# Optimization experiments

Measured on AMD Instinct MI355X. Metric: run time of the kernel, lower is better.

Reference implementation:

```python
import jax, jax.numpy as jnp
import numpy as np

NUM_HEADS = 4
LN_EPS = 1e-5


def setup_inputs() -> dict:
    key = jax.random.key(0)
    B, S, D = 4, 2048, 1024
    H = NUM_HEADS
    hd = D // H
    ks = jax.random.split(key, 8)
    s = 1.0 / np.sqrt(hd)
    inp = {
        "embeddings": jax.random.normal(ks[0], (B, S, D), dtype=jnp.float32),
        # per-head Q/K/V projection weights (torch Linear weight layout [out,in])
        "Wq": jax.random.normal(ks[1], (H, hd, hd), dtype=jnp.float32) * s,
        "Wk": jax.random.normal(ks[2], (H, hd, hd), dtype=jnp.float32) * s,
        "Wv": jax.random.normal(ks[3], (H, hd, hd), dtype=jnp.float32) * s,
        # lens bias scalars: causal, intent, temporal, normative (init values from module)
        "bias_scalars": jnp.array([0.1, 0.15, 0.05, 0.2], dtype=jnp.float32),
        "Wo_w": jax.random.normal(ks[4], (D, D), dtype=jnp.float32) / np.sqrt(D),
        "Wo_b": jnp.zeros((D,), dtype=jnp.float32),
        "ln_g": jnp.ones((D,), dtype=jnp.float32),
        "ln_b": jnp.zeros((D,), dtype=jnp.float32),
    }
    return inp


def _legal_biases(x, bias_scalars):
    """x: [B,H,S,hd] per-head embeddings. Returns stacked bias [B,H,S,S]."""
    B, H, S, hd = x.shape
    # head 0: CAUSAL -> strictly upper triangular mask * causal_bias
    causal = jnp.triu(jnp.ones((S, S), dtype=x.dtype), k=1)  # [S,S]
    b0 = causal[None] * bias_scalars[0]                      # [1,S,S] -> bcast B
    b0 = jnp.broadcast_to(b0, (B, S, S))
    # head 1: INTENTIONALITY -> outer product of embedding norms, global-mean threshold
    mag1 = jnp.linalg.norm(x[:, 1], axis=-1)                 # [B,S]
    intent = mag1[:, :, None] * mag1[:, None, :]             # [B,S,S]
    b1 = (intent > intent.mean()).astype(x.dtype) * bias_scalars[1]
    # head 2: TEMPORAL -> exp(-|i-j|/S)
    pos = jnp.arange(S, dtype=x.dtype)
    prox = jnp.exp(-jnp.abs(pos[:, None] - pos[None, :]) / S)  # [S,S]
    b2 = jnp.broadcast_to(prox[None] * bias_scalars[2], (B, S, S))
    # head 3: NORMATIVE -> outer product of last feature, > 0.5 threshold
    v3 = x[:, 3, :, -1]                                      # [B,S]
    viol = v3[:, :, None] * v3[:, None, :]                   # [B,S,S]
    b3 = (viol > 0.5).astype(x.dtype) * bias_scalars[3]
    return jnp.stack([b0, b1, b2, b3], axis=1)               # [B,H,S,S]


def _forward(embeddings, Wq, Wk, Wv, bias_scalars, Wo_w, Wo_b, ln_g, ln_b):
    B, S, D = embeddings.shape
    H = NUM_HEADS
    hd = D // H
    x = embeddings.reshape(B, S, H, hd).transpose(0, 2, 1, 3)     # [B,H,S,hd]
    # torch Linear: y = x @ W.T
    Q = jnp.einsum('bhsd,hed->bhse', x, Wq)
    K = jnp.einsum('bhsd,hed->bhse', x, Wk)
    V = jnp.einsum('bhsd,hed->bhse', x, Wv)
    scores = jnp.einsum('bhse,bhte->bhst', Q, K) / np.sqrt(hd)    # [B,H,S,S]
    scores = scores + _legal_biases(x, bias_scalars)
    weights = jax.nn.softmax(scores, axis=-1)                     # [B,H,S,S]
    attended = jnp.einsum('bhst,bhte->bhse', weights, V)          # [B,H,S,hd]
    concat = attended.transpose(0, 2, 1, 3).reshape(B, S, D)      # head order = concat order
    out = concat @ Wo_w.T + Wo_b
    # layer_norm(out + embeddings)
    y = out + embeddings
    mu = y.mean(axis=-1, keepdims=True)
    var = ((y - mu) ** 2).mean(axis=-1, keepdims=True)
    output = (y - mu) / jnp.sqrt(var + LN_EPS) * ln_g + ln_b      # [B,S,D]
    average_weights = weights.mean(axis=1)                        # [B,S,S]
    guilt = jax.nn.softmax(average_weights.sum(axis=-1), axis=-1) # [B,S]
    return output, average_weights, guilt


def reference(embeddings, Wq, Wk, Wv, bias_scalars, Wo_w, Wo_b, ln_g, ln_b):
    return _forward(embeddings, Wq, Wk, Wv, bias_scalars, Wo_w, Wo_b, ln_g, ln_b)
```

## Files before the change

kernel.cpp:

```cpp
#include <hip/hip_runtime.h>
#include <hip/hip_bf16.h>
#include <math.h>

#define S_ 2048
#define D_ 1024
#define H_ 4
#define HD_ 256
#define B_ 4

typedef __hip_bfloat16 bf16;
typedef short s16x8 __attribute__((ext_vector_type(8)));
typedef short s16x4 __attribute__((ext_vector_type(4)));
typedef float f32x4 __attribute__((ext_vector_type(4)));

#define GLOAD16(g, l)                                             \
    __builtin_amdgcn_global_load_lds(                             \
        (const __attribute__((address_space(1))) void*)(g),       \
        (__attribute__((address_space(3))) void*)(l), 16, 0, 0)

#define PLOAD(dst, p)                                             \
    asm volatile("global_load_dwordx4 %0, %1, off"                \
                 : "=&v"(dst) : "v"(p) : "memory")

static __device__ inline short bfb(float x) {
    bf16 t = __float2bfloat16(x);
    short s;
    __builtin_memcpy(&s, &t, 2);
    return s;
}

template <int MODE>
__global__ __launch_bounds__(256) void mfma_nt(
    int K,
    const bf16* __restrict__ A, int lda, long sA_b, long sA_h,
    const bf16* __restrict__ Bm, int ldb, long sB_b, long sB_h,
    void* __restrict__ Cp, int ldc, long sC_b, long sC_h,
    int zdiv, int bbase,
    const double* __restrict__ mag1d, const double* __restrict__ v3d,
    const double* __restrict__ meand, const float* __restrict__ bias_sc)
{
    __shared__ __align__(16) short As[128 * 32];
    __shared__ __align__(16) short Bs[128 * 32];

    const int tid = threadIdx.x;
    const int w = tid >> 6, lane = tid & 63;
    const int srow = lane >> 2;
    const int scol = (((lane & 3) ^ (srow & 3)) << 3);
    const int quad = lane >> 4, r = lane & 15;
    const int qx = quad ^ (r & 3);
    const int wr = (w >> 1) * 64, wc = (w & 1) * 64;
    const int zb = blockIdx.z / zdiv, zh = blockIdx.z % zdiv;

    const bf16* Ap = A + (size_t)zb * sA_b + (size_t)zh * sA_h +
                     (size_t)blockIdx.y * 128 * lda;
    const bf16* Bp = Bm + (size_t)zb * sB_b + (size_t)zh * sB_h +
                     (size_t)blockIdx.x * 128 * ldb;

    f32x4 acc[4][4] = {};

    for (int k0 = 0; k0 < K; k0 += 32) {
        if (k0) __syncthreads();
#pragma unroll
        for (int l = 0; l < 2; l++) {
            GLOAD16(Ap + (size_t)(w * 32 + l * 16 + srow) * lda + (k0 + scol),
                    &As[(w * 32 + l * 16) * 32]);
            GLOAD16(Bp + (size_t)(w * 32 + l * 16 + srow) * ldb + (k0 + scol),
                    &Bs[(w * 32 + l * 16) * 32]);
        }
        __syncthreads();

        s16x8 af[4], bfv[4];
        const s16x8* A8 = (const s16x8*)As;
        const s16x8* B8 = (const s16x8*)Bs;
#pragma unroll
        for (int i = 0; i < 4; i++) af[i] = A8[(wr + i * 16 + r) * 4 + qx];
#pragma unroll
        for (int j = 0; j < 4; j++) bfv[j] = B8[(wc + j * 16 + r) * 4 + qx];
#pragma unroll
        for (int i = 0; i < 4; i++)
#pragma unroll
            for (int j = 0; j < 4; j++)
                acc[i][j] = __builtin_amdgcn_mfma_f32_16x16x32_bf16(
                    af[i], bfv[j], acc[i][j], 0, 0, 0);
    }

    const int row0 = blockIdx.y * 128 + wr + quad * 4;
    const int col0 = blockIdx.x * 128 + wc + r;

    if (MODE == 0) {
        float* C = (float*)Cp + (size_t)zb * sC_b + (size_t)zh * sC_h;
#pragma unroll
        for (int i = 0; i < 4; i++)
#pragma unroll
            for (int j = 0; j < 4; j++)
#pragma unroll
                for (int p = 0; p < 4; p++)
                    C[(size_t)(row0 + i * 16 + p) * ldc + (col0 + j * 16)] = acc[i][j][p];
    } else if (MODE == 1) {
        bf16* C = (bf16*)Cp + (size_t)zb * sC_b + (size_t)zh * sC_h;
#pragma unroll
        for (int i = 0; i < 4; i++)
#pragma unroll
            for (int j = 0; j < 4; j++)
#pragma unroll
                for (int p = 0; p < 4; p++)
                    C[(size_t)(row0 + i * 16 + p) * ldc + (col0 + j * 16)] =
                        __float2bfloat16(acc[i][j][p]);
    } else {
        float* C = (float*)Cp + (size_t)zb * sC_b + (size_t)zh * sC_h;
        const int h = zh;
        const int bbatch = bbase + zb;
        const float bsc = bias_sc[h];
        if (h == 0) {
#pragma unroll
            for (int i = 0; i < 4; i++)
#pragma unroll
                for (int j = 0; j < 4; j++)
#pragma unroll
                    for (int p = 0; p < 4; p++) {
                        const int rr = row0 + i * 16 + p, c = col0 + j * 16;
                        C[(size_t)rr * ldc + c] = acc[i][j][p] + ((c > rr) ? bsc : 0.0f);
                    }
        } else if (h == 2) {
#pragma unroll
            for (int i = 0; i < 4; i++)
#pragma unroll
                for (int j = 0; j < 4; j++)
#pragma unroll
                    for (int p = 0; p < 4; p++) {
                        const int rr = row0 + i * 16 + p, c = col0 + j * 16;
                        int d = c - rr; d = d < 0 ? -d : d;
                        C[(size_t)rr * ldc + c] =
                            acc[i][j][p] + bsc * expf(-(float)d * (1.0f / 2048.0f));
                    }
        } else {
            const double* src = (h == 1) ? mag1d : v3d;
            const double thr = (h == 1) ? meand[0] : 0.5;
            double rv[16], cv[4];
#pragma unroll
            for (int i = 0; i < 4; i++)
#pragma unroll
                for (int p = 0; p < 4; p++)
                    rv[i * 4 + p] = src[(size_t)bbatch * S_ + row0 + i * 16 + p];
#pragma unroll
            for (int j = 0; j < 4; j++)
                cv[j] = src[(size_t)bbatch * S_ + col0 + j * 16];
#pragma unroll
            for (int i = 0; i < 4; i++)
#pragma unroll
                for (int j = 0; j < 4; j++)
#pragma unroll
                    for (int p = 0; p < 4; p++) {
                        const int rr = row0 + i * 16 + p, c = col0 + j * 16;
                        C[(size_t)rr * ldc + c] =
                            acc[i][j][p] + ((rv[i * 4 + p] * cv[j] > thr) ? bsc : 0.0f);
                    }
        }
    }
}

__global__ __launch_bounds__(512) void mfma_pv(const bf16* __restrict__ Pm,
                                               const bf16* __restrict__ Vt,
                                               bf16* __restrict__ Cc) {
    __shared__ __align__(16) short Lv[3][8192];

    const int tid = threadIdx.x;
    const int w = tid >> 6, lane = tid & 63;
    const int quad = lane >> 4, r = lane & 15;
    const int qx = quad ^ (r & 3);
    const int wr = (w >> 2) * 64, wc = (w & 3) * 64;

    const int bid = blockIdx.x;
    const int bh = (bid & 7) * 2 + ((bid >> 3) >> 4);
    const int rb = (bid >> 3) & 15;
    const int b = bh >> 2, h = bh & 3;

    const bf16* Ap = Pm + ((size_t)bh * S_ + (size_t)rb * 128) * S_;
    const bf16* Bp = Vt + (size_t)(h * B_ + b) * HD_ * S_;

    const int srow = tid >> 2;
    const int scol = (((tid & 3) ^ (srow & 3)) << 3);

    f32x4 acc[4][4] = {};

    const bf16* q0 = Ap + (size_t)(wr + 0 * 16 + r) * S_ + quad * 8;
    const bf16* q1 = Ap + (size_t)(wr + 1 * 16 + r) * S_ + quad * 8;
    const bf16* q2 = Ap + (size_t)(wr + 2 * 16 + r) * S_ + quad * 8;
    const bf16* q3 = Ap + (size_t)(wr + 3 * 16 + r) * S_ + quad * 8;

    s16x8 paA[4], paB[4];

    auto stageV = [&](int bs, int t) {
        const int k0 = t * 32;
        GLOAD16(Bp + (size_t)srow * S_ + (k0 + scol), &Lv[bs][w * 512]);
        GLOAD16(Bp + (size_t)(128 + srow) * S_ + (k0 + scol),
                &Lv[bs][4096 + w * 512]);
    };
    auto compute = [&](int bs, const s16x8* pa) {
        const s16x8* B8 = (const s16x8*)&Lv[bs][0];
        s16x8 bfv[4];
#pragma unroll
        for (int j = 0; j < 4; j++) bfv[j] = B8[(wc + j * 16 + r) * 4 + qx];
        __builtin_amdgcn_s_setprio(1);
#pragma unroll
        for (int i = 0; i < 4; i++)
#pragma unroll
            for (int j = 0; j < 4; j++)
                acc[i][j] = __builtin_amdgcn_mfma_f32_16x16x32_bf16(
                    pa[i], bfv[j], acc[i][j], 0, 0, 0);
        __builtin_amdgcn_s_setprio(0);
    };

#define PV_WAITB(N)                                           \
    asm volatile("s_waitcnt vmcnt(" #N ")" ::: "memory");     \
    __builtin_amdgcn_s_barrier();                             \
    __builtin_amdgcn_sched_barrier(0);

    stageV(0, 0);
    PLOAD(paA[0], q0); PLOAD(paA[1], q1); PLOAD(paA[2], q2); PLOAD(paA[3], q3);
    stageV(1, 1);
    PLOAD(paB[0], q0 + 32); PLOAD(paB[1], q1 + 32);
    PLOAD(paB[2], q2 + 32); PLOAD(paB[3], q3 + 32);
    q0 += 64; q1 += 64; q2 += 64; q3 += 64;

    int cb = 0;
#pragma unroll 1
    for (int t = 0; t < 62; t += 2) {
        PV_WAITB(6);
        {
            int sb = cb + 2; if (sb >= 3) sb -= 3;
            stageV(sb, t + 2);
        }
        compute(cb, paA);
        PLOAD(paA[0], q0); PLOAD(paA[1], q1); PLOAD(paA[2], q2); PLOAD(paA[3], q3);
        q0 += 32; q1 += 32; q2 += 32; q3 += 32;
        cb = (cb == 2) ? 0 : cb + 1;
        PV_WAITB(6);
        {
            int sb = cb + 2; if (sb >= 3) sb -= 3;
            stageV(sb, t + 3);
        }
        compute(cb, paB);
        PLOAD(paB[0], q0); PLOAD(paB[1], q1); PLOAD(paB[2], q2); PLOAD(paB[3], q3);
        q0 += 32; q1 += 32; q2 += 32; q3 += 32;
        cb = (cb == 2) ? 0 : cb + 1;
    }
    PV_WAITB(6);
    compute(cb, paA);
    cb = (cb == 2) ? 0 : cb + 1;
    PV_WAITB(0);
    compute(cb, paB);
#undef PV_WAITB

    const int row0 = rb * 128 + wr + quad * 4;
    const int col0 = h * HD_ + wc + r;
    bf16* C = Cc + (size_t)b * S_ * D_;
#pragma unroll
    for (int i = 0; i < 4; i++)
#pragma unroll
        for (int j = 0; j < 4; j++)
#pragma unroll
            for (int p = 0; p < 4; p++)
                C[(size_t)(row0 + i * 16 + p) * D_ + col0 + j * 16] =
                    __float2bfloat16(acc[i][j][p]);
}

__global__ __launch_bounds__(256) void cvt_bf16(const float* __restrict__ in,
                                                bf16* __restrict__ out, int n,
                                                float scale) {
    const size_t i0 = ((size_t)blockIdx.x * 256 + threadIdx.x) * 4;
    if (i0 + 3 < (size_t)n) {
        const float4 v = *(const float4*)(in + i0);
        out[i0 + 0] = __float2bfloat16(v.x * scale);
        out[i0 + 1] = __float2bfloat16(v.y * scale);
        out[i0 + 2] = __float2bfloat16(v.z * scale);
        out[i0 + 3] = __float2bfloat16(v.w * scale);
    }
}

__global__ __launch_bounds__(256) void transpose_v(const bf16* __restrict__ in,
                                                   bf16* __restrict__ out) {
    const int h = blockIdx.z / B_, b = blockIdx.z % B_;
    const int e0 = blockIdx.x * 64, s0 = blockIdx.y * 64;
    __shared__ short t[64][66];
    const int tid = threadIdx.x;
    const int rr = tid >> 2;
    const int cc = (tid & 3) << 4;
    const bf16* ip = in + (((size_t)h * B_ * S_) + (size_t)b * S_ + s0) * HD_ + e0;
    const s16x8 v0 = *(const s16x8*)(ip + (size_t)rr * HD_ + cc);
    const s16x8 v1 = *(const s16x8*)(ip + (size_t)rr * HD_ + cc + 8);
#pragma unroll
    for (int i = 0; i < 8; i++) {
        t[rr][cc + i] = v0[i];
        t[rr][cc + 8 + i] = v1[i];
    }
    __syncthreads();
    bf16* op = out + (((size_t)h * B_ + b) * HD_ + e0 + rr) * S_ + s0 + cc;
    s16x8 o0, o1;
#pragma unroll
    for (int i = 0; i < 8; i++) {
        o0[i] = t[cc + i][rr];
        o1[i] = t[cc + 8 + i][rr];
    }
    *(s16x8*)op = o0;
    *(s16x8*)(op + 8) = o1;
}

__global__ __launch_bounds__(256) void prep_kernel(const float* __restrict__ emb,
                                                   double* __restrict__ mag1d,
                                                   double* __restrict__ v3d) {
    const long row = blockIdx.x;
    const int tid = threadIdx.x;
    const float x = emb[row * D_ + 256 + tid];
    __shared__ double red[256];
    red[tid] = (double)x * (double)x;
    __syncthreads();
    for (int off = 128; off > 0; off >>= 1) {
        if (tid < off) red[tid] += red[tid + off];
        __syncthreads();
    }
    if (tid == 0) {
        mag1d[row] = sqrt(red[0]);
        v3d[row] = (double)emb[row * D_ + 1023];
    }
}

__global__ __launch_bounds__(256) void mean_kernel(const double* __restrict__ mag1d,
                                                   double* __restrict__ meand) {
    const int tid = threadIdx.x;
    __shared__ double red[256];
    double acc = 0.0;
    for (int b = 0; b < B_; b++) {
        double ss = 0.0;
        for (int i = tid; i < S_; i += 256) ss += mag1d[(long)b * S_ + i];
        __syncthreads();
        red[tid] = ss;
        __syncthreads();
        for (int off = 128; off > 0; off >>= 1) {
            if (tid < off) red[tid] += red[tid + off];
            __syncthreads();
        }
        if (tid == 0) {
            const double rb = red[0] / (double)S_;
            acc += rb * rb;
        }
        __syncthreads();
    }
    if (tid == 0) meand[0] = acc / (double)B_;
}

__global__ __launch_bounds__(256) void softmax_fused(
    const float* __restrict__ scores, bf16* __restrict__ P, long p_h, int p_row,
    float* __restrict__ avgw, float* __restrict__ rowsum) {
    const int s = blockIdx.x, tid = threadIdx.x;
    __shared__ float red[256];
    float wacc[8] = {0, 0, 0, 0, 0, 0, 0, 0};
    for (int h = 0; h < H_; h++) {
        const float* rp = scores + ((size_t)h * S_ + s) * S_;
        bf16* pp = P + (size_t)h * p_h + (size_t)s * p_row;
        const float4 va = ((const float4*)rp)[tid];
        const float4 vb = ((const float4*)rp)[256 + tid];
        float v[8] = {va.x, va.y, va.z, va.w, vb.x, vb.y, vb.z, vb.w};
        float m = -1e30f;
#pragma unroll
        for (int i = 0; i < 8; i++) m = fmaxf(m, v[i]);
        red[tid] = m;
        __syncthreads();
        for (int off = 128; off > 0; off >>= 1) {
            if (tid < off) red[tid] = fmaxf(red[tid], red[tid + off]);
            __syncthreads();
        }
        m = red[0];
        __syncthreads();
        float sum = 0.0f;
#pragma unroll
        for (int i = 0; i < 8; i++) {
            v[i] = expf(v[i] - m);
            sum += v[i];
        }
        red[tid] = sum;
        __syncthreads();
        for (int off = 128; off > 0; off >>= 1) {
            if (tid < off) red[tid] += red[tid + off];
            __syncthreads();
        }
        const float inv = 1.0f / red[0];
        __syncthreads();
        s16x4 pk0, pk1;
#pragma unroll
        for (int j = 0; j < 4; j++) {
            const float w0 = v[j] * inv;
            const float w1 = v[4 + j] * inv;
            pk0[j] = bfb(w0);
            pk1[j] = bfb(w1);
            wacc[j] += w0;
            wacc[4 + j] += w1;
        }
        *(s16x4*)(pp + (size_t)tid * 4) = pk0;
        *(s16x4*)(pp + 1024 + (size_t)tid * 4) = pk1;
    }
    float4 a0, a1;
    a0.x = wacc[0] * 0.25f; a0.y = wacc[1] * 0.25f;
    a0.z = wacc[2] * 0.25f; a0.w = wacc[3] * 0.25f;
    a1.x = wacc[4] * 0.25f; a1.y = wacc[5] * 0.25f;
    a1.z = wacc[6] * 0.25f; a1.w = wacc[7] * 0.25f;
    float* ar = avgw + (size_t)s * S_;
    ((float4*)ar)[tid] = a0;
    ((float4*)ar)[256 + tid] = a1;
    const float asum = a0.x + a0.y + a0.z + a0.w + a1.x + a1.y + a1.z + a1.w;
    red[tid] = asum;
    __syncthreads();
    for (int off = 128; off > 0; off >>= 1) {
        if (tid < off) red[tid] += red[tid + off];
        __syncthreads();
    }
    if (tid == 0) rowsum[s] = red[0];
}

__global__ __launch_bounds__(256) void ln_kernel(float* __restrict__ out,
                                                 const float* __restrict__ emb,
                                                 const float* __restrict__ wob,
                                                 const float* __restrict__ g,
                                                 const float* __restrict__ beta) {
    const long row = blockIdx.x;
    float* o = out + row * D_;
    const float* e = emb + row * D_;
    const int tid = threadIdx.x;
    __shared__ float red[256];
    const float4 vo = ((const float4*)o)[tid];
    const float4 vw = ((const float4*)wob)[tid];
    const float4 ve = ((const float4*)e)[tid];
    float v[4] = {vo.x + vw.x + ve.x, vo.y + vw.y + ve.y,
                  vo.z + vw.z + ve.z, vo.w + vw.w + ve.w};
    red[tid] = v[0] + v[1] + v[2] + v[3];
    __syncthreads();
    for (int off = 128; off > 0; off >>= 1) {
        if (tid < off) red[tid] += red[tid + off];
        __syncthreads();
    }
    const float mu = red[0] * (1.0f / 1024.0f);
    __syncthreads();
    float vs = 0.0f;
#pragma unroll
    for (int i = 0; i < 4; i++) {
        const float d = v[i] - mu;
        vs += d * d;
    }
    red[tid] = vs;
    __syncthreads();
    for (int off = 128; off > 0; off >>= 1) {
        if (tid < off) red[tid] += red[tid + off];
        __syncthreads();
    }
    const float var = red[0] * (1.0f / 1024.0f);
    const float inv = 1.0f / sqrtf(var + 1e-5f);
    const float4 g4 = ((const float4*)g)[tid];
    const float4 b4 = ((const float4*)beta)[tid];
    float4 r4;
    r4.x = (v[0] - mu) * inv * g4.x + b4.x;
    r4.y = (v[1] - mu) * inv * g4.y + b4.y;
    r4.z = (v[2] - mu) * inv * g4.z + b4.z;
    r4.w = (v[3] - mu) * inv * g4.w + b4.w;
    ((float4*)o)[tid] = r4;
}

__global__ __launch_bounds__(256) void guilt_kernel(const float* __restrict__ rowsum,
                                                    float* __restrict__ guilt) {
    const int b = blockIdx.x, tid = threadIdx.x;
    const float* r = rowsum + (long)b * S_;
    float* gq = guilt + (long)b * S_;
    __shared__ float red[256];
    float v[8];
    float m = -1e30f;
#pragma unroll
    for (int i = 0; i < 8; i++) {
        v[i] = r[tid + 256 * i];
        m = fmaxf(m, v[i]);
    }
    red[tid] = m;
    __syncthreads();
    for (int off = 128; off > 0; off >>= 1) {
        if (tid < off) red[tid] = fmaxf(red[tid], red[tid + off]);
        __syncthreads();
    }
    m = red[0];
    __syncthreads();
    float sum = 0.0f;
#pragma unroll
    for (int i = 0; i < 8; i++) {
        v[i] = expf(v[i] - m);
        sum += v[i];
    }
    red[tid] = sum;
    __syncthreads();
    for (int off = 128; off > 0; off >>= 1) {
        if (tid < off) red[tid] += red[tid + off];
        __syncthreads();
    }
    const float inv = 1.0f / red[0];
#pragma unroll
    for (int i = 0; i < 8; i++) gq[tid + 256 * i] = v[i] * inv;
}

extern "C" void kernel_launch(void* const* d_in, const int* in_sizes, int n_in,
                              void* d_out, int out_size, void* d_ws, size_t ws_size,
                              hipStream_t stream) {
    const float* emb = (const float*)d_in[0];
    const float* Wq = (const float*)d_in[1];
    const float* Wk = (const float*)d_in[2];
    const float* Wv = (const float*)d_in[3];
    const float* bias_sc = (const float*)d_in[4];
    const float* Wo_w = (const float*)d_in[5];
    const float* Wo_b = (const float*)d_in[6];
    const float* ln_g = (const float*)d_in[7];
    const float* ln_bt = (const float*)d_in[8];

    char* ws = (char*)d_ws;
    size_t off = 0;
    auto alloc = [&](size_t bytes) {
        size_t o = off;
        off = (off + bytes + 255) & ~(size_t)255;
        return o;
    };
    bf16* embb = (bf16*)(ws + alloc((size_t)B_ * S_ * D_ * 2));
    bf16* concat = embb;
    bf16* Qm = (bf16*)(ws + alloc((size_t)H_ * B_ * S_ * HD_ * 2));
    bf16* Km = (bf16*)(ws + alloc((size_t)H_ * B_ * S_ * HD_ * 2));
    bf16* Vtb = (bf16*)(ws + alloc((size_t)H_ * B_ * HD_ * S_ * 2));
    bf16* Wqb = (bf16*)(ws + alloc((size_t)H_ * HD_ * HD_ * 2));
    bf16* Wkb = (bf16*)(ws + alloc((size_t)H_ * HD_ * HD_ * 2));
    bf16* Wvb = (bf16*)(ws + alloc((size_t)H_ * HD_ * HD_ * 2));
    bf16* Wob = (bf16*)(ws + alloc((size_t)D_ * D_ * 2));
    double* mag1d = (double*)(ws + alloc((size_t)B_ * S_ * 8));
    double* v3d = (double*)(ws + alloc((size_t)B_ * S_ * 8));
    double* meand = (double*)(ws + alloc(256));
    float* rowsum = (float*)(ws + alloc((size_t)B_ * S_ * 4));
    float* scores = (float*)(ws + alloc((size_t)H_ * S_ * S_ * 4));
    bf16* Vraw = (bf16*)scores;
    bf16* P = (bf16*)(ws + off);
    const size_t need_batched = off + (size_t)B_ * H_ * S_ * S_ * 2;
    const bool batched = ws_size >= need_batched;

    float* outp = (float*)d_out;
    float* avgw = outp + (size_t)B_ * S_ * D_;
    float* guilt = avgw + (size_t)B_ * S_ * S_;

    cvt_bf16<<<(B_ * S_ * D_) / 1024, 256, 0, stream>>>(emb, embb, B_ * S_ * D_, 1.0f);
    cvt_bf16<<<(H_ * HD_ * HD_) / 1024, 256, 0, stream>>>(Wq, Wqb, H_ * HD_ * HD_, 0.0625f);
    cvt_bf16<<<(H_ * HD_ * HD_) / 1024, 256, 0, stream>>>(Wk, Wkb, H_ * HD_ * HD_, 1.0f);
    cvt_bf16<<<(H_ * HD_ * HD_) / 1024, 256, 0, stream>>>(Wv, Wvb, H_ * HD_ * HD_, 1.0f);
    cvt_bf16<<<(D_ * D_) / 1024, 256, 0, stream>>>(Wo_w, Wob, D_ * D_, 1.0f);

    prep_kernel<<<B_ * S_, 256, 0, stream>>>(emb, mag1d, v3d);
    mean_kernel<<<1, 256, 0, stream>>>(mag1d, meand);

    {
        const dim3 g(HD_ / 128, (B_ * S_) / 128, H_);
        const long sQ = (long)B_ * S_ * HD_;
        mfma_nt<1><<<g, 256, 0, stream>>>(HD_, embb, D_, 0, HD_,
                                          Wqb, HD_, 0, (long)HD_ * HD_,
                                          Qm, HD_, 0, sQ, H_, 0,
                                          nullptr, nullptr, nullptr, nullptr);
        mfma_nt<1><<<g, 256, 0, stream>>>(HD_, embb, D_, 0, HD_,
                                          Wkb, HD_, 0, (long)HD_ * HD_,
                                          Km, HD_, 0, sQ, H_, 0,
                                          nullptr, nullptr, nullptr, nullptr);
        mfma_nt<1><<<g, 256, 0, stream>>>(HD_, embb, D_, 0, HD_,
                                          Wvb, HD_, 0, (long)HD_ * HD_,
                                          Vraw, HD_, 0, sQ, H_, 0,
                                          nullptr, nullptr, nullptr, nullptr);
    }
    transpose_v<<<dim3(HD_ / 64, S_ / 64, H_ * B_), 256, 0, stream>>>(Vraw, Vtb);

    for (int b = 0; b < B_; b++) {
        mfma_nt<3><<<dim3(S_ / 128, S_ / 128, H_), 256, 0, stream>>>(
            HD_,
            Qm + (size_t)b * S_ * HD_, HD_, 0, (long)B_ * S_ * HD_,
            Km + (size_t)b * S_ * HD_, HD_, 0, (long)B_ * S_ * HD_,
            scores, S_, 0, (long)S_ * S_,
            H_, b, mag1d, v3d, meand, bias_sc);
        if (batched) {
            softmax_fused<<<S_, 256, 0, stream>>>(
                scores, P + (size_t)b * H_ * S_ * S_, (long)S_ * S_, S_,
                avgw + (size_t)b * S_ * S_, rowsum + (size_t)b * S_);
        } else {
            softmax_fused<<<S_, 256, 0, stream>>>(
                scores, (bf16*)scores, 2L * S_ * S_, 2 * S_,
                avgw + (size_t)b * S_ * S_, rowsum + (size_t)b * S_);
            mfma_nt<1><<<dim3(HD_ / 128, S_ / 128, H_), 256, 0, stream>>>(
                S_,
                (const bf16*)scores, 2 * S_, 0, 2L * S_ * S_,
                Vtb + (size_t)b * HD_ * S_, S_, 0, (long)B_ * HD_ * S_,
                concat + (size_t)b * S_ * D_, D_, 0, HD_,
                H_, 0, nullptr, nullptr, nullptr, nullptr);
        }
    }
    if (batched) {
        mfma_pv<<<256, 512, 0, stream>>>(P, Vtb, concat);
    }

    mfma_nt<0><<<dim3(D_ / 128, (B_ * S_) / 128, 1), 256, 0, stream>>>(
        D_, concat, D_, 0, 0, Wob, D_, 0, 0, outp, D_, 0, 0,
        1, 0, nullptr, nullptr, nullptr, nullptr);

    ln_kernel<<<B_ * S_, 256, 0, stream>>>(outp, emb, Wo_b, ln_g, ln_bt);
    guilt_kernel<<<B_, 256, 0, stream>>>(rowsum, guilt);
}
```

Baseline: 536.7 us.

## Add triple-buffered LDS pipeline to GEMM and deepen PV kernel staging to six buffers

The generic NT GEMM kernel moves from a single LDS buffer with two barriers per k-step to a three-stage ring of async global-to-LDS loads, one waitcnt/barrier per step, and MFMA priority raising. The PV kernel stops loading P fragments straight into registers. It now stages both P and V tiles through LDS in a six-deep ring with five tiles in flight. The goal is to hide global memory latency behind MFMA work, at the cost of more LDS per block (about 144KB for PV), which may limit occupancy.

```diff
diff --git a/kernel.cpp b/kernel.cpp
--- a/kernel.cpp
+++ b/kernel.cpp
@@ -18,9 +18,10 @@
         (const __attribute__((address_space(1))) void*)(g),       \
         (__attribute__((address_space(3))) void*)(l), 16, 0, 0)
 
-#define PLOAD(dst, p)                                             \
-    asm volatile("global_load_dwordx4 %0, %1, off"                \
-                 : "=&v"(dst) : "v"(p) : "memory")
+#define WAITB(N)                                              \
+    asm volatile("s_waitcnt vmcnt(" #N ")" ::: "memory");     \
+    __builtin_amdgcn_s_barrier();                             \
+    __builtin_amdgcn_sched_barrier(0);
 
 static __device__ inline short bfb(float x) {
     bf16 t = __float2bfloat16(x);
@@ -39,8 +40,8 @@
     const double* __restrict__ mag1d, const double* __restrict__ v3d,
     const double* __restrict__ meand, const float* __restrict__ bias_sc)
 {
-    __shared__ __align__(16) short As[128 * 32];
-    __shared__ __align__(16) short Bs[128 * 32];
+    __shared__ __align__(16) short As[3][128 * 32];
+    __shared__ __align__(16) short Bs[3][128 * 32];
 
     const int tid = threadIdx.x;
     const int w = tid >> 6, lane = tid & 63;
@@ -58,31 +59,50 @@
 
     f32x4 acc[4][4] = {};
 
-    for (int k0 = 0; k0 < K; k0 += 32) {
-        if (k0) __syncthreads();
+    auto stage = [&](int bs, int k0) {
 #pragma unroll
         for (int l = 0; l < 2; l++) {
             GLOAD16(Ap + (size_t)(w * 32 + l * 16 + srow) * lda + (k0 + scol),
-                    &As[(w * 32 + l * 16) * 32]);
+                    &As[bs][(w * 32 + l * 16) * 32]);
             GLOAD16(Bp + (size_t)(w * 32 + l * 16 + srow) * ldb + (k0 + scol),
-                    &Bs[(w * 32 + l * 16) * 32]);
-        }
-        __syncthreads();
-
+                    &Bs[bs][(w * 32 + l * 16) * 32]);
+        }
+    };
+    auto compute = [&](int bs) {
+        const s16x8* A8 = (const s16x8*)&As[bs][0];
+        const s16x8* B8 = (const s16x8*)&Bs[bs][0];
         s16x8 af[4], bfv[4];
-        const s16x8* A8 = (const s16x8*)As;
-        const s16x8* B8 = (const s16x8*)Bs;
 #pragma unroll
         for (int i = 0; i < 4; i++) af[i] = A8[(wr + i * 16 + r) * 4 + qx];
 #pragma unroll
         for (int j = 0; j < 4; j++) bfv[j] = B8[(wc + j * 16 + r) * 4 + qx];
+        __builtin_amdgcn_s_setprio(1);
 #pragma unroll
         for (int i = 0; i < 4; i++)
 #pragma unroll
             for (int j = 0; j < 4; j++)
                 acc[i][j] = __builtin_amdgcn_mfma_f32_16x16x32_bf16(
                     af[i], bfv[j], acc[i][j], 0, 0, 0);
-    }
+        __builtin_amdgcn_s_setprio(0);
+    };
+
+    const int NT = K >> 5;
+    stage(0, 0);
+    stage(1, 32);
+    int cb = 0;
+#pragma unroll 1
+    for (int t = 0; t < NT - 2; ++t) {
+        WAITB(4);
+        int sb = cb + 2; if (sb >= 3) sb -= 3;
+        stage(sb, (t + 2) * 32);
+        compute(cb);
+        cb = (cb == 2) ? 0 : cb + 1;
+    }
+    WAITB(4);
+    compute(cb);
+    cb = (cb == 2) ? 0 : cb + 1;
+    WAITB(0);
+    compute(cb);
 
     const int row0 = blockIdx.y * 128 + wr + quad * 4;
     const int col0 = blockIdx.x * 128 + wc + r;
@@ -162,7 +182,7 @@
 __global__ __launch_bounds__(512) void mfma_pv(const bf16* __restrict__ Pm,
                                                const bf16* __restrict__ Vt,
                                                bf16* __restrict__ Cc) {
-    __shared__ __align__(16) short Lv[3][8192];
+    __shared__ __align__(16) short L[6][12288];
 
     const int tid = threadIdx.x;
     const int w = tid >> 6, lane = tid & 63;
@@ -180,25 +200,23 @@
 
     const int srow = tid >> 2;
     const int scol = (((tid & 3) ^ (srow & 3)) << 3);
+    const int wbase = w * 512;
 
     f32x4 acc[4][4] = {};
 
-    const bf16* q0 = Ap + (size_t)(wr + 0 * 16 + r) * S_ + quad * 8;
-    const bf16* q1 = Ap + (size_t)(wr + 1 * 16 + r) * S_ + quad * 8;
-    const bf16* q2 = Ap + (size_t)(wr + 2 * 16 + r) * S_ + quad * 8;
-    const bf16* q3 = Ap + (size_t)(wr + 3 * 16 + r) * S_ + quad * 8;
-
-    s16x8 paA[4], paB[4];
-
-    auto stageV = [&](int bs, int t) {
+    auto stage = [&](int bs, int t) {
+        short* sb = &L[bs][0];
         const int k0 = t * 32;
-        GLOAD16(Bp + (size_t)srow * S_ + (k0 + scol), &Lv[bs][w * 512]);
-        GLOAD16(Bp + (size_t)(128 + srow) * S_ + (k0 + scol),
-                &Lv[bs][4096 + w * 512]);
+        GLOAD16(Ap + (size_t)srow * S_ + (k0 + scol), sb + wbase);
+        GLOAD16(Bp + (size_t)srow * S_ + (k0 + scol), sb + 4096 + wbase);
+        GLOAD16(Bp + (size_t)(128 + srow) * S_ + (k0 + scol), sb + 8192 + wbase);
     };
-    auto compute = [&](int bs, const s16x8* pa) {
-        const s16x8* B8 = (const s16x8*)&Lv[bs][0];
-        s16x8 bfv[4];
+    auto compute = [&](int bs) {
+        const s16x8* A8 = (const s16x8*)&L[bs][0];
+        const s16x8* B8 = (const s16x8*)&L[bs][4096];
+        s16x8 af[4], bfv[4];
+#pragma unroll
+        for (int i = 0; i < 4; i++) af[i] = A8[(wr + i * 16 + r) * 4 + qx];
 #pragma unroll
         for (int j = 0; j < 4; j++) bfv[j] = B8[(wc + j * 16 + r) * 4 + qx];
         __builtin_amdgcn_s_setprio(1);
@@ -207,50 +225,26 @@
 #pragma unroll
             for (int j = 0; j < 4; j++)
                 acc[i][j] = __builtin_amdgcn_mfma_f32_16x16x32_bf16(
-                    pa[i], bfv[j], acc[i][j], 0, 0, 0);
+                    af[i], bfv[j], acc[i][j], 0, 0, 0);
         __builtin_amdgcn_s_setprio(0);
     };
 
-#define PV_WAITB(N)                                           \
-    asm volatile("s_waitcnt vmcnt(" #N ")" ::: "memory");     \
-    __builtin_amdgcn_s_barrier();                             \
-    __builtin_amdgcn_sched_barrier(0);
-
-    stageV(0, 0);
-    PLOAD(paA[0], q0); PLOAD(paA[1], q1); PLOAD(paA[2], q2); PLOAD(paA[3], q3);
-    stageV(1, 1);
-    PLOAD(paB[0], q0 + 32); PLOAD(paB[1], q1 + 32);
-    PLOAD(paB[2], q2 + 32); PLOAD(paB[3], q3 + 32);
-    q0 += 64; q1 += 64; q2 += 64; q3 += 64;
-
-    int cb = 0;
+    stage(0, 0); stage(1, 1); stage(2, 2); stage(3, 3); stage(4, 4);
+
+    int cb = 0, sn = 5;
 #pragma unroll 1
-    for (int t = 0; t < 62; t += 2) {
-        PV_WAITB(6);
-        {
-            int sb = cb + 2; if (sb >= 3) sb -= 3;
-            stageV(sb, t + 2);
-        }
-        compute(cb, paA);
-        PLOAD(paA[0], q0); PLOAD(paA[1], q1); PLOAD(paA[2], q2); PLOAD(paA[3], q3);
-        q0 += 32; q1 += 32; q2 += 32; q3 += 32;
-        cb = (cb == 2) ? 0 : cb + 1;
-        PV_WAITB(6);
-        {
-            int sb = cb + 2; if (sb >= 3) sb -= 3;
-            stageV(sb, t + 3);
-        }
-        compute(cb, paB);
-        PLOAD(paB[0], q0); PLOAD(paB[1], q1); PLOAD(paB[2], q2); PLOAD(paB[3], q3);
-        q0 += 32; q1 += 32; q2 += 32; q3 += 32;
-        cb = (cb == 2) ? 0 : cb + 1;
-    }
-    PV_WAITB(6);
-    compute(cb, paA);
-    cb = (cb == 2) ? 0 : cb + 1;
-    PV_WAITB(0);
-    compute(cb, paB);
-#undef PV_WAITB
+    for (int t = 0; t < 59; ++t) {
+        WAITB(12);
+        stage(sn, t + 5);
+        compute(cb);
+        cb = (cb == 5) ? 0 : cb + 1;
+        sn = (sn == 5) ? 0 : sn + 1;
+    }
+    WAITB(12); compute(cb); cb = (cb == 5) ? 0 : cb + 1;
+    WAITB(9);  compute(cb); cb = (cb == 5) ? 0 : cb + 1;
+    WAITB(6);  compute(cb); cb = (cb == 5) ? 0 : cb + 1;
+    WAITB(3);  compute(cb); cb = (cb == 5) ? 0 : cb + 1;
+    WAITB(0);  compute(cb);
 
     const int row0 = rb * 128 + wr + quad * 4;
     const int col0 = h * HD_ + wc + r;
```

New measurement: 510.2 us. -4.9%, faster.
